# Kernel optimization log

Measured on AMD Instinct MI355X. Metric: run time of the kernel, lower is better.

The kernel has to match this reference:

```python
import jax, jax.numpy as jnp
import numpy as np

FILTER_FACTOR = 10  # init kwarg


def median_filter2d(x, k, padding="REFLECT", constant_values=0.0):
    """Faithful port of tfa.image.median_filter2d for NHWC float input.

    tfa pads with pad_top=(k-1)//2, pad_bottom=k-1-pad_top (same for width),
    extracts k*k patches per pixel/channel, and takes the element that
    tf.nn.top_k(patches, area//2+1)[..., -1] yields, i.e. the value at
    ascending-sorted index (area-1)//2.
    """
    B, H, W, C = x.shape
    pt = (k - 1) // 2
    pb = k - 1 - pt
    mode = {"REFLECT": "reflect", "SYMMETRIC": "symmetric", "CONSTANT": "constant"}[padding]
    if mode == "constant":
        xp = jnp.pad(x, ((0, 0), (pt, pb), (pt, pb), (0, 0)), mode=mode,
                     constant_values=constant_values)
    else:
        xp = jnp.pad(x, ((0, 0), (pt, pb), (pt, pb), (0, 0)), mode=mode)
    # Gather sliding windows via advanced indexing (vectorized, no data loops).
    ih = jnp.arange(H)[:, None] + jnp.arange(k)[None, :]  # (H, k)
    iw = jnp.arange(W)[:, None] + jnp.arange(k)[None, :]  # (W, k)
    rows = xp[:, ih]                 # (B, H, k, Wp, C)
    patches = rows[:, :, :, iw]      # (B, H, k, W, k, C)
    patches = patches.transpose(0, 1, 3, 5, 2, 4).reshape(B, H, W, C, k * k)
    area = k * k
    med = jnp.sort(patches, axis=-1)[..., (area - 1) // 2]  # (B, H, W, C)
    return med


def setup_inputs() -> dict:
    key = jax.random.key(0)
    k1, k2 = jax.random.split(key)
    inputs = jax.random.uniform(k1, (2, 224, 224, 3), dtype=jnp.float32)
    # layer draws blend ~ U[0.1, 1.0)
    blend = jax.random.uniform(k2, (1,), dtype=jnp.float32) * 0.9 + 0.1
    return {"inputs": inputs, "blend": blend}


def reference(inputs, blend):
    # training=True path: median filter then tfa.image.blend(filtered, inputs, blend)
    # blend(image1, image2, f) = image1 + f * (image2 - image1)
    k = inputs.shape[1] // FILTER_FACTOR  # height // filter_factor
    filt = median_filter2d(inputs, k, padding="REFLECT", constant_values=0.0)
    f = blend[0]
    return filt + f * (inputs - filt)
```

## Files before the change

### kernel.cpp

```cpp
#include <hip/hip_runtime.h>


#define HH 224
#define WW 224
#define CHN 3
#define KK 22
#define PT 10
#define AREA (KK * KK)
#define RANK 242
#define PXW 8
#define XGS (WW / PXW)
#define DT 2

#define INFF  __int_as_float(0x7f800000)
#define NINFF __int_as_float(0xff800000)

__device__ __forceinline__ int reflect224(int g) {
    int a = abs(g);
    return min(a, 2 * (HH - 1) - a);
}

__device__ __forceinline__ int count8(const float v[8], float t) {
    int c = 0;
#pragma unroll
    for (int i = 0; i < 8; ++i)
        c += __popcll(__ballot(v[i] < t));
    return c;
}

__device__ __forceinline__ void gather(float v[8], const float* __restrict__ img,
                                       const int voff[8], int lane, int x) {
    if (x >= PT && x <= WW - 1 - (KK - 1 - PT)) {
        const float* base = img + (x - PT) * CHN;
#pragma unroll
        for (int i = 0; i < 8; ++i) v[i] = base[voff[i]];
    } else {
#pragma unroll
        for (int i = 0; i < 8; ++i) {
            int s   = i * 64 + lane;
            int se  = min(s, AREA - 1);
            int row = se / KK;
            int col = se - row * KK;
            int gy672 = voff[i] - col * CHN;
            int gx = reflect224(x - PT + col);
            v[i] = img[gy672 + gx * CHN];
        }
    }
    v[7] = (lane < AREA - 448) ? v[7] : INFF;
}

__global__ __launch_bounds__(256)
void median_blend_kernel(const float* __restrict__ in,
                         const float* __restrict__ blend,
                         float* __restrict__ out) {
    const int lane = threadIdx.x & 63;
    const int wid  = threadIdx.x >> 6;
    const int wg = blockIdx.x * 4 + wid;
    const int xg = wg % XGS;
    const int t1 = wg / XGS;
    const int y  = t1 % HH;
    const int t2 = t1 / HH;
    const int c  = t2 % CHN;
    const int b  = t2 / CHN;

    const float f = blend[0];
    const float* img  = in  + (size_t)b * (HH * WW * CHN) + c;
    float*       outp = out + (size_t)b * (HH * WW * CHN) + c;

    int voff[8];
#pragma unroll
    for (int i = 0; i < 8; ++i) {
        int s   = i * 64 + lane;
        int se  = min(s, AREA - 1);
        int row = se / KK;
        int col = se - row * KK;
        int gy  = reflect224(y - PT + row);
        voff[i] = gy * (WW * CHN) + col * CHN;
    }

    const int x0 = xg * PXW;
    float tprev = 0.5f;

#pragma unroll 1
    for (int j = 0; j < PXW; j += 2) {
        const int xA = x0 + j;
        const int xB = xA + 1;

        float vA[8], vB[8];
        gather(vA, img, voff, lane, xA);
        gather(vB, img, voff, lane, xB);

        float tA = tprev, tB = tprev;
        int CA = count8(vA, tA);
        int CB = count8(vB, tB);
        float loA = 0.0f, hiA = 1.0f, loB = 0.0f, hiB = 1.0f;
        int cloA = 0, chiA = AREA, cloB = 0, chiB = AREA;
        bool actA = true, actB = true;
#pragma unroll 1
        for (int it = 0; it < 16 && (actA || actB); ++it) {
            if (actA) {
                int d = CA - RANK;
                if (d >= -DT && d <= DT) actA = false;
                else {
                    if (d > 0) { hiA = tA; chiA = CA; }
                    else       { loA = tA; cloA = CA; }
                    float tn = loA + (hiA - loA) * (float)(RANK - cloA) *
                               __builtin_amdgcn_rcpf((float)(chiA - cloA));
                    if (!(tn > loA && tn < hiA)) {
                        tn = 0.5f * (loA + hiA);
                        if (!(tn > loA && tn < hiA)) actA = false;
                    }
                    if (actA) { tA = tn; CA = count8(vA, tA); }
                }
            }
            if (actB) {
                int d = CB - RANK;
                if (d >= -DT && d <= DT) actB = false;
                else {
                    if (d > 0) { hiB = tB; chiB = CB; }
                    else       { loB = tB; cloB = CB; }
                    float tn = loB + (hiB - loB) * (float)(RANK - cloB) *
                               __builtin_amdgcn_rcpf((float)(chiB - cloB));
                    if (!(tn > loB && tn < hiB)) {
                        tn = 0.5f * (loB + hiB);
                        if (!(tn > loB && tn < hiB)) actB = false;
                    }
                    if (actB) { tB = tn; CB = count8(vB, tB); }
                }
            }
        }

        const int dA = CA - RANK, dB = CB - RANK;
        const bool topA = (dA >= 0), topB = (dB >= 0);
        int eA = topA ? dA + 1 : -dA;
        int eB = topB ? dB + 1 : -dB;
        const int sgnA = topA ? 0 : 0x80000000;
        const int sgnB = topB ? 0 : 0x80000000;
#pragma unroll
        for (int i = 0; i < 8; ++i) {
            bool ltA = vA[i] < tA;
            float sA = __int_as_float(__float_as_int(vA[i]) ^ sgnA);
            vA[i] = (ltA == topA) ? sA : NINFF;
            bool ltB = vB[i] < tB;
            float sB = __int_as_float(__float_as_int(vB[i]) ^ sgnB);
            vB[i] = (ltB == topB) ? sB : NINFF;
        }

        float medA = tA, medB = tB;
        bool doneA = false, doneB = false;
#pragma unroll 1
        for (int r = 0; r < 300 && !(doneA && doneB); ++r) {
            float mA = fmaxf(fmaxf(fmaxf(vA[0], vA[1]), fmaxf(vA[2], vA[3])),
                             fmaxf(fmaxf(vA[4], vA[5]), fmaxf(vA[6], vA[7])));
            float mB = fmaxf(fmaxf(fmaxf(vB[0], vB[1]), fmaxf(vB[2], vB[3])),
                             fmaxf(fmaxf(vB[4], vB[5]), fmaxf(vB[6], vB[7])));
#pragma unroll
            for (int off = 32; off > 0; off >>= 1) {
                mA = fmaxf(mA, __shfl_xor(mA, off, 64));
                mB = fmaxf(mB, __shfl_xor(mB, off, 64));
            }
            if (!doneA) {
                int q = 0;
#pragma unroll
                for (int i = 0; i < 8; ++i)
                    q += __popcll(__ballot(vA[i] == mA));
                if (eA <= q) {
                    medA = __int_as_float(__float_as_int(mA) ^ sgnA);
                    doneA = true;
                } else {
                    eA -= q;
#pragma unroll
                    for (int i = 0; i < 8; ++i)
                        vA[i] = (vA[i] == mA) ? NINFF : vA[i];
                }
            }
            if (!doneB) {
                int q = 0;
#pragma unroll
                for (int i = 0; i < 8; ++i)
                    q += __popcll(__ballot(vB[i] == mB));
                if (eB <= q) {
                    medB = __int_as_float(__float_as_int(mB) ^ sgnB);
                    doneB = true;
                } else {
                    eB -= q;
#pragma unroll
                    for (int i = 0; i < 8; ++i)
                        vB[i] = (vB[i] == mB) ? NINFF : vB[i];
                }
            }
        }
        tprev = medB;

        const float xcA = img[y * (WW * CHN) + xA * CHN];
        const float xcB = img[y * (WW * CHN) + xB * CHN];
        if (lane == 0) {
            outp[y * (WW * CHN) + xA * CHN] = medA + f * (xcA - medA);
            outp[y * (WW * CHN) + xB * CHN] = medB + f * (xcB - medB);
        }
    }
}

extern "C" void kernel_launch(void* const* d_in, const int* in_sizes, int n_in,
                              void* d_out, int out_size, void* d_ws, size_t ws_size,
                              hipStream_t stream) {
    const float* in    = (const float*)d_in[0];
    const float* blend = (const float*)d_in[1];
    float* out = (float*)d_out;

    const int nwaves  = 2 * CHN * HH * XGS;
    const int nblocks = nwaves / 4;
    median_blend_kernel<<<nblocks, 256, 0, stream>>>(in, blend, out);
}
```

Measured before the change: 162.9 us.

## Process four pixels per batch with multi-threshold bracketing before secant search

```diff
diff --git a/kernel.cpp b/kernel.cpp
--- a/kernel.cpp
+++ b/kernel.cpp
@@ -82,121 +82,165 @@
     float tprev = 0.5f;
 
 #pragma unroll 1
-    for (int j = 0; j < PXW; j += 2) {
-        const int xA = x0 + j;
-        const int xB = xA + 1;
-
-        float vA[8], vB[8];
-        gather(vA, img, voff, lane, xA);
-        gather(vB, img, voff, lane, xB);
-
-        float tA = tprev, tB = tprev;
-        int CA = count8(vA, tA);
-        int CB = count8(vB, tB);
-        float loA = 0.0f, hiA = 1.0f, loB = 0.0f, hiB = 1.0f;
-        int cloA = 0, chiA = AREA, cloB = 0, chiB = AREA;
-        bool actA = true, actB = true;
+    for (int q = 0; q < 2; ++q) {
+        const int xq = x0 + q * 4;
+
+        float v[4][8];
+#pragma unroll
+        for (int p = 0; p < 4; ++p)
+            gather(v[p], img, voff, lane, xq + p);
+
+        const float dl = (q == 0) ? 0.020f : 0.012f;
+        const float tc = tprev;
+        int Cl[4][5];
+#pragma unroll
+        for (int p = 0; p < 4; ++p)
+#pragma unroll
+            for (int k = 0; k < 5; ++k)
+                Cl[p][k] = count8(v[p], tc + (float)(k - 2) * dl);
+
+        float t[4], lo[4], hi[4];
+        int C[4], clo[4], chi[4];
+#pragma unroll
+        for (int p = 0; p < 4; ++p) {
+            float l = 0.0f, h = 1.0f;
+            int cl = 0, ch = AREA;
+#pragma unroll
+            for (int k = 0; k < 5; ++k) {
+                float tk = tc + (float)(k - 2) * dl;
+                if (Cl[p][k] < RANK && tk > l) { l = tk; cl = Cl[p][k]; }
+            }
+#pragma unroll
+            for (int k = 0; k < 5; ++k) {
+                float tk = tc + (float)(k - 2) * dl;
+                if (Cl[p][k] >= RANK && tk < h) { h = tk; ch = Cl[p][k]; }
+            }
+            float tn = l + (h - l) * (float)(RANK - cl) *
+                       __builtin_amdgcn_rcpf((float)(ch - cl));
+            if (!(tn > l && tn < h)) tn = 0.5f * (l + h);
+            if (!(tn > l && tn < h)) tn = l;
+            t[p] = tn; lo[p] = l; hi[p] = h; clo[p] = cl; chi[p] = ch;
+        }
+#pragma unroll
+        for (int p = 0; p < 4; ++p)
+            C[p] = count8(v[p], t[p]);
+
+        float med[4];
+
+#pragma unroll
+        for (int pr = 0; pr < 2; ++pr) {
+            const int A = 2 * pr, B = 2 * pr + 1;
+
+            float tA = t[A], tB = t[B];
+            int   CA = C[A], CB = C[B];
+            float loA = lo[A], hiA = hi[A], loB = lo[B], hiB = hi[B];
+            int   cloA = clo[A], chiA = chi[A], cloB = clo[B], chiB = chi[B];
+            bool actA = true, actB = true;
 #pragma unroll 1
-        for (int it = 0; it < 16 && (actA || actB); ++it) {
-            if (actA) {
-                int d = CA - RANK;
-                if (d >= -DT && d <= DT) actA = false;
-                else {
-                    if (d > 0) { hiA = tA; chiA = CA; }
-                    else       { loA = tA; cloA = CA; }
-                    float tn = loA + (hiA - loA) * (float)(RANK - cloA) *
-                               __builtin_amdgcn_rcpf((float)(chiA - cloA));
-                    if (!(tn > loA && tn < hiA)) {
-                        tn = 0.5f * (loA + hiA);
-                        if (!(tn > loA && tn < hiA)) actA = false;
-                    }
-                    if (actA) { tA = tn; CA = count8(vA, tA); }
-                }
-            }
-            if (actB) {
-                int d = CB - RANK;
-                if (d >= -DT && d <= DT) actB = false;
-                else {
-                    if (d > 0) { hiB = tB; chiB = CB; }
-                    else       { loB = tB; cloB = CB; }
-                    float tn = loB + (hiB - loB) * (float)(RANK - cloB) *
-                               __builtin_amdgcn_rcpf((float)(chiB - cloB));
-                    if (!(tn > loB && tn < hiB)) {
-                        tn = 0.5f * (loB + hiB);
-                        if (!(tn > loB && tn < hiB)) actB = false;
-                    }
-                    if (actB) { tB = tn; CB = count8(vB, tB); }
-                }
-            }
-        }
-
-        const int dA = CA - RANK, dB = CB - RANK;
-        const bool topA = (dA >= 0), topB = (dB >= 0);
-        int eA = topA ? dA + 1 : -dA;
-        int eB = topB ? dB + 1 : -dB;
-        const int sgnA = topA ? 0 : 0x80000000;
-        const int sgnB = topB ? 0 : 0x80000000;
-#pragma unroll
-        for (int i = 0; i < 8; ++i) {
-            bool ltA = vA[i] < tA;
-            float sA = __int_as_float(__float_as_int(vA[i]) ^ sgnA);
-            vA[i] = (ltA == topA) ? sA : NINFF;
-            bool ltB = vB[i] < tB;
-            float sB = __int_as_float(__float_as_int(vB[i]) ^ sgnB);
-            vB[i] = (ltB == topB) ? sB : NINFF;
-        }
-
-        float medA = tA, medB = tB;
-        bool doneA = false, doneB = false;
+            for (int it = 0; it < 8 && (actA || actB); ++it) {
+                if (actA) {
+                    int d = CA - RANK;
+                    if (d >= -DT && d <= DT) actA = false;
+                    else {
+                        if (d > 0) { hiA = tA; chiA = CA; }
+                        else       { loA = tA; cloA = CA; }
+                        float tn = loA + (hiA - loA) * (float)(RANK - cloA) *
+                                   __builtin_amdgcn_rcpf((float)(chiA - cloA));
+                        if (!(tn > loA && tn < hiA)) {
+                            tn = 0.5f * (loA + hiA);
+                            if (!(tn > loA && tn < hiA)) actA = false;
+                        }
+                        if (actA) { tA = tn; CA = count8(v[A], tA); }
+                    }
+                }
+                if (actB) {
+                    int d = CB - RANK;
+                    if (d >= -DT && d <= DT) actB = false;
+                    else {
+                        if (d > 0) { hiB = tB; chiB = CB; }
+                        else       { loB = tB; cloB = CB; }
+                        float tn = loB + (hiB - loB) * (float)(RANK - cloB) *
+                                   __builtin_amdgcn_rcpf((float)(chiB - cloB));
+                        if (!(tn > loB && tn < hiB)) {
+                            tn = 0.5f * (loB + hiB);
+                            if (!(tn > loB && tn < hiB)) actB = false;
+                        }
+                        if (actB) { tB = tn; CB = count8(v[B], tB); }
+                    }
+                }
+            }
+
+            const int dA = CA - RANK, dB = CB - RANK;
+            const bool topA = (dA >= 0), topB = (dB >= 0);
+            int eA = topA ? dA + 1 : -dA;
+            int eB = topB ? dB + 1 : -dB;
+            const int sgnA = topA ? 0 : 0x80000000;
+            const int sgnB = topB ? 0 : 0x80000000;
+#pragma unroll
+            for (int i = 0; i < 8; ++i) {
+                bool ltA = v[A][i] < tA;
+                float sA = __int_as_float(__float_as_int(v[A][i]) ^ sgnA);
+                v[A][i] = (ltA == topA) ? sA : NINFF;
+                bool ltB = v[B][i] < tB;
+                float sB = __int_as_float(__float_as_int(v[B][i]) ^ sgnB);
+                v[B][i] = (ltB == topB) ? sB : NINFF;
+            }
+
+            float medA = tA, medB = tB;
+            bool doneA = false, doneB = false;
 #pragma unroll 1
-        for (int r = 0; r < 300 && !(doneA && doneB); ++r) {
-            float mA = fmaxf(fmaxf(fmaxf(vA[0], vA[1]), fmaxf(vA[2], vA[3])),
-                             fmaxf(fmaxf(vA[4], vA[5]), fmaxf(vA[6], vA[7])));
-            float mB = fmaxf(fmaxf(fmaxf(vB[0], vB[1]), fmaxf(vB[2], vB[3])),
-                             fmaxf(fmaxf(vB[4], vB[5]), fmaxf(vB[6], vB[7])));
-#pragma unroll
-            for (int off = 32; off > 0; off >>= 1) {
-                mA = fmaxf(mA, __shfl_xor(mA, off, 64));
-                mB = fmaxf(mB, __shfl_xor(mB, off, 64));
-            }
-            if (!doneA) {
-                int q = 0;
-#pragma unroll
-                for (int i = 0; i < 8; ++i)
-                    q += __popcll(__ballot(vA[i] == mA));
-                if (eA <= q) {
-                    medA = __int_as_float(__float_as_int(mA) ^ sgnA);
-                    doneA = true;
-                } else {
-                    eA -= q;
+            for (int r = 0; r < 300 && !(doneA && doneB); ++r) {
+                float mA = fmaxf(fmaxf(fmaxf(v[A][0], v[A][1]), fmaxf(v[A][2], v[A][3])),
+                                 fmaxf(fmaxf(v[A][4], v[A][5]), fmaxf(v[A][6], v[A][7])));
+                float mB = fmaxf(fmaxf(fmaxf(v[B][0], v[B][1]), fmaxf(v[B][2], v[B][3])),
+                                 fmaxf(fmaxf(v[B][4], v[B][5]), fmaxf(v[B][6], v[B][7])));
+#pragma unroll
+                for (int off = 32; off > 0; off >>= 1) {
+                    mA = fmaxf(mA, __shfl_xor(mA, off, 64));
+                    mB = fmaxf(mB, __shfl_xor(mB, off, 64));
+                }
+                if (!doneA) {
+                    int qq = 0;
 #pragma unroll
                     for (int i = 0; i < 8; ++i)
-                        vA[i] = (vA[i] == mA) ? NINFF : vA[i];
-                }
-            }
-            if (!doneB) {
-                int q = 0;
-#pragma unroll
-                for (int i = 0; i < 8; ++i)
-                    q += __popcll(__ballot(vB[i] == mB));
-                if (eB <= q) {
-                    medB = __int_as_float(__float_as_int(mB) ^ sgnB);
-                    doneB = true;
-                } else {
-                    eB -= q;
+                        qq += __popcll(__ballot(v[A][i] == mA));
+                    if (eA <= qq) {
+                        medA = __int_as_float(__float_as_int(mA) ^ sgnA);
+                        doneA = true;
+                    } else {
+                        eA -= qq;
+#pragma unroll
+                        for (int i = 0; i < 8; ++i)
+                            v[A][i] = (v[A][i] == mA) ? NINFF : v[A][i];
+                    }
+                }
+                if (!doneB) {
+                    int qq = 0;
 #pragma unroll
                     for (int i = 0; i < 8; ++i)
-                        vB[i] = (vB[i] == mB) ? NINFF : vB[i];
-                }
-            }
-        }
-        tprev = medB;
-
-        const float xcA = img[y * (WW * CHN) + xA * CHN];
-        const float xcB = img[y * (WW * CHN) + xB * CHN];
-        if (lane == 0) {
-            outp[y * (WW * CHN) + xA * CHN] = medA + f * (xcA - medA);
-            outp[y * (WW * CHN) + xB * CHN] = medB + f * (xcB - medB);
+                        qq += __popcll(__ballot(v[B][i] == mB));
+                    if (eB <= qq) {
+                        medB = __int_as_float(__float_as_int(mB) ^ sgnB);
+                        doneB = true;
+                    } else {
+                        eB -= qq;
+#pragma unroll
+                        for (int i = 0; i < 8; ++i)
+                            v[B][i] = (v[B][i] == mB) ? NINFF : v[B][i];
+                    }
+                }
+            }
+            med[A] = medA;
+            med[B] = medB;
+        }
+        tprev = med[3];
+
+#pragma unroll
+        for (int p = 0; p < 4; ++p) {
+            const int x = xq + p;
+            const float xc = img[y * (WW * CHN) + x * CHN];
+            if (lane == 0)
+                outp[y * (WW * CHN) + x * CHN] = med[p] + f * (xc - med[p]);
         }
     }
 }
```

Result: slower. 234.0 us (+43.7%).
